# Kernel optimization log

Measured on AMD Instinct MI355X. Metric: run time of the kernel, lower is better.

The kernel has to match this reference:

```python
import jax, jax.numpy as jnp
import numpy as np
from jax import lax

B, T_Y, T_X = 16, 1600, 400
MEL_C, TXT_C, MAS_C = 80, 512, 384
HID = MAS_C * 2          # SwiGLUConvFFN hidden width (mas_channels*2)
NEG = -1e9


def setup_inputs() -> dict:
    key = jax.random.key(0)
    ks = jax.random.split(key, 20)
    p = lambda k, s: jax.random.normal(k, s, jnp.float32) * 0.02
    return {
        "mel_hidden_states": jax.random.normal(ks[0], (B, T_Y, MEL_C), jnp.float32),
        "text_hidden_states": jax.random.normal(ks[1], (B, T_X, TXT_C), jnp.float32),
        # mel SwiGLU conv-FFN (kernel 5): in->2*HID, gate, HID->MAS_C
        "mel_w1": p(ks[2], (2 * HID, MEL_C, 5)), "mel_b1": jnp.zeros((2 * HID,), jnp.float32),
        "mel_w2": p(ks[3], (MAS_C, HID, 5)),     "mel_b2": jnp.zeros((MAS_C,), jnp.float32),
        # text SwiGLU conv-FFN (kernel 3)
        "txt_w1": p(ks[4], (2 * HID, TXT_C, 3)), "txt_b1": jnp.zeros((2 * HID,), jnp.float32),
        "txt_w2": p(ks[5], (MAS_C, HID, 3)),     "txt_b2": jnp.zeros((MAS_C,), jnp.float32),
        # SimpleAttention query/key projections (value proj does not affect returned outputs)
        "wq": p(ks[6], (MAS_C, MAS_C)), "bq": jnp.zeros((MAS_C,), jnp.float32),
        "wk": p(ks[7], (MAS_C, MAS_C)), "bk": jnp.zeros((MAS_C,), jnp.float32),
        "x_lens": jax.random.randint(ks[8], (B,), T_X // 2, T_X + 1).astype(jnp.int32),
        "y_lens": jax.random.randint(ks[9], (B,), T_Y // 2, T_Y + 1).astype(jnp.int32),
    }


def _conv_ffn(x, pad_mask, w1, b1, w2, b2):
    """SwiGLU/ReGLU conv FFN. x:(B,T,C), pad_mask:(B,T) True=padded."""
    keep = (~pad_mask)[:, None, :].astype(x.dtype)          # (B,1,T)
    h = jnp.transpose(x, (0, 2, 1)) * keep                  # (B,C,T)
    dn = ("NCH", "OIH", "NCH")
    h = lax.conv_general_dilated(h, w1, (1,), "SAME", dimension_numbers=dn) + b1[None, :, None]
    a, g = jnp.split(h, 2, axis=1)
    h = a * jax.nn.relu(g) * keep                           # relugt gating
    h = lax.conv_general_dilated(h, w2, (1,), "SAME", dimension_numbers=dn) + b2[None, :, None]
    return jnp.transpose(h * keep, (0, 2, 1))               # (B,T,out)


def _mas_single(logp, t_x, t_y):
    """Glow-TTS maximum_path for one item. logp:(T_X,T_Y). Returns hard path (T_X,T_Y)."""
    xi = jnp.arange(T_X)
    yi = jnp.arange(T_Y)
    valid = (xi[:, None] < t_x) & (yi[None, :] < t_y) & (xi[:, None] <= yi[None, :])
    lp = jnp.where(valid, logp, NEG)

    def fstep(prev, col):                                   # prev:(T_X,), col:(T_X,)
        shifted = jnp.concatenate([jnp.full((1,), NEG, prev.dtype), prev[:-1]])
        cur = col + jnp.maximum(prev, shifted)
        return cur, cur

    init = jnp.where(xi == 0, 0.0, NEG).astype(logp.dtype)
    _, v = lax.scan(fstep, init, lp.T)                      # v:(T_Y,T_X) DP table

    def bstep(x, y):                                        # backtrack from y=T_Y-1 down
        active = y < t_y
        row = (xi == x) & active
        vp = v[y - 1]
        dec = (x > 0) & ((x == y) | (vp[jnp.maximum(x - 1, 0)] > vp[x]))
        new_x = jnp.where(active & (y > 0) & dec, x - 1, x)
        return new_x, row

    _, rows = lax.scan(bstep, t_x - 1, jnp.arange(T_Y - 1, -1, -1))
    return rows[::-1].T.astype(jnp.float32)                 # (T_X,T_Y)


def _safe_log(t, eps=1e-6):
    return jnp.nan_to_num(jnp.log(t + eps), nan=eps)


def reference(mel_hidden_states, text_hidden_states,
              mel_w1, mel_b1, mel_w2, mel_b2,
              txt_w1, txt_b1, txt_w2, txt_b2,
              wq, bq, wk, bk, x_lens, y_lens):
    x_mask = jnp.arange(T_X)[None, :] >= x_lens[:, None]    # (B,T_X) True=padded
    y_mask = jnp.arange(T_Y)[None, :] >= y_lens[:, None]    # (B,T_Y)

    text_proj = _conv_ffn(text_hidden_states, x_mask, txt_w1, txt_b1, txt_w2, txt_b2)
    mel_proj = _conv_ffn(mel_hidden_states, y_mask, mel_w1, mel_b1, mel_w2, mel_b2)

    q = mel_proj @ wq.T + bq                                # (B,T_Y,D)
    k = text_proj @ wk.T + bk                               # (B,T_X,D)
    scores = jnp.einsum("byd,bxd->byx", q, k) / (MAS_C ** 0.5)
    # expand_masks: mask==0 only where query AND key are both padded (faithful to source)
    both_pad = y_mask[:, :, None] & x_mask[:, None, :]
    scores = jnp.where(both_pad, jnp.float32(-1e-9), scores)
    attn_w = jax.nn.softmax(scores, axis=-1)                # (B,T_Y,T_X)

    avg_attn = attn_w[:, None]                              # (B,1,T_Y,T_X)
    attn_logprob = _safe_log(avg_attn)

    mas_in = jnp.transpose(attn_logprob[:, 0], (0, 2, 1))   # (B,T_X,T_Y)
    attn_hard = lax.stop_gradient(jax.vmap(_mas_single)(mas_in, x_lens, y_lens))
    attn_hard_dur = attn_hard.sum(2)                        # (B,T_X)
    return avg_attn, attn_logprob, attn_hard, attn_hard_dur
```

## Files before the change

kernel.cpp:

```cpp
#include <hip/hip_runtime.h>
#include <cstdint>

#define B 16
#define TY 1600
#define TX 400
#define MAS 384
#define HID 768
#define NEGV -1e9f

typedef __bf16 bf16x8 __attribute__((ext_vector_type(8)));
typedef float  f32x4  __attribute__((ext_vector_type(4)));
typedef float  f32x16 __attribute__((ext_vector_type(16)));

__device__ __forceinline__ f32x4 mfma16(bf16x8 a, bf16x8 b, f32x4 c) {
  return __builtin_amdgcn_mfma_f32_16x16x32_bf16(a, b, c, 0, 0, 0);
}
__device__ __forceinline__ f32x16 mfma32(bf16x8 a, bf16x8 b, f32x16 c) {
  return __builtin_amdgcn_mfma_f32_32x32x16_bf16(a, b, c, 0, 0, 0);
}

__global__ void split_pad_k(const float* __restrict__ in, __bf16* __restrict__ oh,
                            __bf16* __restrict__ ol, int CIN, int CINP, long n) {
  long i = (long)blockIdx.x * 256 + threadIdx.x;
  if (i >= n) return;
  long row = i / CINP; int ci = (int)(i - row * CINP);
  float v = (ci < CIN) ? in[row * CIN + ci] : 0.f;
  __bf16 h = (__bf16)v;
  oh[i] = h; ol[i] = (__bf16)(v - (float)h);
}

__global__ void wsplit_k(const float* __restrict__ w, __bf16* __restrict__ oh,
                         __bf16* __restrict__ ol, int CIN, int K_, int CINP, long n) {
  long i = (long)blockIdx.x * 256 + threadIdx.x;
  if (i >= n) return;
  long kdspan = (long)K_ * CINP;
  long nn = i / kdspan; int kd = (int)(i - nn * kdspan);
  int k = kd / CINP, ci = kd - k * CINP;
  float v = (ci < CIN) ? w[(nn * CIN + ci) * K_ + k] : 0.f;
  __bf16 h = (__bf16)v;
  oh[i] = h; ol[i] = (__bf16)(v - (float)h);
}

__global__ void tsplit_k(const float* __restrict__ in, __bf16* __restrict__ oh,
                         __bf16* __restrict__ ol, int JTOT, long n) {
  long i = (long)blockIdx.x * 256 + threadIdx.x;
  if (i >= n) return;
  int m = (int)(i / JTOT), j = (int)(i - (long)m * JTOT);
  float v = in[i];
  long o = (long)j * 384 + m;
  __bf16 h = (__bf16)v;
  oh[o] = h; ol[o] = (__bf16)(v - (float)h);
}

__global__ void fold_bias_k(const float* __restrict__ wq, const float* __restrict__ b,
                            float* __restrict__ o) {
  int n = threadIdx.x;
  float s = 0.f;
  for (int m = 0; m < 384; ++m) s = fmaf(wq[n * 384 + m], b[m], s);
  o[n] = s;
}

template<int KK>
__global__ __launch_bounds__(256)
void fold_mfma(const __bf16* __restrict__ xh, const __bf16* __restrict__ xl,
               const __bf16* __restrict__ wh, const __bf16* __restrict__ wl,
               __bf16* __restrict__ oh, __bf16* __restrict__ ol)
{
  constexpr int CINP = 384, ROWS = 64, STRIDE = 65;
  __shared__ float4 xs[8 * STRIDE];
  const int t0 = blockIdx.x * 64, n0 = blockIdx.y * 128;
  const int tid = threadIdx.x, wn = tid >> 6, lane = tid & 63;
  const int lr = lane & 15, lg = lane >> 4;
  const f32x4 Z4 = {0.f, 0.f, 0.f, 0.f};
  f32x4 acc[4][2];
  #pragma unroll
  for (int m = 0; m < 4; ++m) { acc[m][0] = Z4; acc[m][1] = Z4; }

  #pragma unroll 1
  for (int ci0 = 0; ci0 < CINP; ci0 += 32) {
    __syncthreads();
    for (int e = tid; e < ROWS * 8; e += 256) {
      int row = e >> 3, sc = e & 7, spl = sc >> 2, cg = sc & 3;
      int t = t0 + row;
      xs[(spl * 4 + cg) * STRIDE + row] =
          *(const float4*)((spl ? xl : xh) + (size_t)t * CINP + ci0 + cg * 8);
    }
    __syncthreads();
    bf16x8 ah[4], al[4];
    #pragma unroll
    for (int mf = 0; mf < 4; ++mf) {
      int row = mf * 16 + lr;
      ah[mf] = *(const bf16x8*)&xs[lg * STRIDE + row];
      al[mf] = *(const bf16x8*)&xs[(4 + lg) * STRIDE + row];
    }
    size_t kd = (size_t)ci0 + lg * 8;
    bf16x8 bh[2], bl[2];
    #pragma unroll
    for (int nf = 0; nf < 2; ++nf) {
      int nc = n0 + wn * 32 + nf * 16 + lr;
      bh[nf] = *(const bf16x8*)(wh + (size_t)nc * 384 + kd);
      bl[nf] = *(const bf16x8*)(wl + (size_t)nc * 384 + kd);
    }
    #pragma unroll
    for (int nf = 0; nf < 2; ++nf)
      #pragma unroll
      for (int mf = 0; mf < 4; ++mf) acc[mf][nf] = mfma16(ah[mf], bh[nf], acc[mf][nf]);
    #pragma unroll
    for (int nf = 0; nf < 2; ++nf)
      #pragma unroll
      for (int mf = 0; mf < 4; ++mf) acc[mf][nf] = mfma16(ah[mf], bl[nf], acc[mf][nf]);
    #pragma unroll
    for (int nf = 0; nf < 2; ++nf)
      #pragma unroll
      for (int mf = 0; mf < 4; ++mf) acc[mf][nf] = mfma16(al[mf], bh[nf], acc[mf][nf]);
  }
  #pragma unroll
  for (int nf = 0; nf < 2; ++nf) {
    int c = n0 + wn * 32 + nf * 16 + lr;
    #pragma unroll
    for (int mf = 0; mf < 4; ++mf) {
      #pragma unroll
      for (int r = 0; r < 4; ++r) {
        int j = t0 + mf * 16 + lg * 4 + r;
        int k = j % KK, ci = j / KK;
        size_t o = (size_t)((((ci >> 4) * KK + k) * 2 + ((ci >> 3) & 1)) * 3072)
                 + (size_t)c * 8 + (ci & 7);
        float v = acc[mf][nf][r];
        __bf16 vh = (__bf16)v;
        oh[o] = vh; ol[o] = (__bf16)(v - (float)vh);
      }
    }
  }
}

template<int CINP, int K, int T>
__global__ __launch_bounds__(256)
void conv1_mfma(const __bf16* __restrict__ xh, const __bf16* __restrict__ xl,
                const __bf16* __restrict__ wh, const __bf16* __restrict__ wl,
                const float* __restrict__ bias, const int* __restrict__ lens,
                __bf16* __restrict__ hh, __bf16* __restrict__ hl)
{
  constexpr int BM = 128, PAD = K / 2, ROWS = BM + K - 1, KD = K * CINP;
  __shared__ float4 xs[8 * ROWS];
  const int b = blockIdx.z, t0 = blockIdx.x * BM, n0 = blockIdx.y * 64;
  const int tid = threadIdx.x, wid = tid >> 6, lane = tid & 63;
  const int wm = wid >> 1, wn = wid & 1, lr = lane & 15, lg = lane >> 4;
  const int len = lens[b];
  const f32x4 Z4 = {0.f, 0.f, 0.f, 0.f};
  f32x4 acc_a[4][2], acc_g[4][2];
  #pragma unroll
  for (int m = 0; m < 4; ++m)
    #pragma unroll
    for (int n = 0; n < 2; ++n) { acc_a[m][n] = Z4; acc_g[m][n] = Z4; }

  #pragma unroll 1
  for (int ci0 = 0; ci0 < CINP; ci0 += 32) {
    __syncthreads();
    for (int e = tid; e < ROWS * 8; e += 256) {
      int row = e >> 3, sc = e & 7, spl = sc >> 2, cg = sc & 3;
      int t = t0 + row - PAD;
      float4 v = {0.f, 0.f, 0.f, 0.f};
      if (t >= 0 && t < len)
        v = *(const float4*)((spl ? xl : xh) + ((size_t)b * T + t) * CINP + ci0 + cg * 8);
      xs[(spl * 4 + cg) * ROWS + row] = v;
    }
    __syncthreads();
    #pragma unroll
    for (int k = 0; k < K; ++k) {
      bf16x8 ah[4], al[4];
      #pragma unroll
      for (int mf = 0; mf < 4; ++mf) {
        int row = wm * 64 + mf * 16 + lr + k;
        ah[mf] = *(const bf16x8*)&xs[lg * ROWS + row];
        al[mf] = *(const bf16x8*)&xs[(4 + lg) * ROWS + row];
      }
      size_t kd = (size_t)k * CINP + ci0 + lg * 8;
      #pragma unroll
      for (int nf = 0; nf < 2; ++nf) {
        int na = n0 + wn * 32 + nf * 16 + lr;
        bf16x8 bah = *(const bf16x8*)(wh + (size_t)na * KD + kd);
        bf16x8 bal = *(const bf16x8*)(wl + (size_t)na * KD + kd);
        bf16x8 bgh = *(const bf16x8*)(wh + (size_t)(na + HID) * KD + kd);
        bf16x8 bgl = *(const bf16x8*)(wl + (size_t)(na + HID) * KD + kd);
        #pragma unroll
        for (int mf = 0; mf < 4; ++mf) {
          acc_a[mf][nf] = mfma16(ah[mf], bah, acc_a[mf][nf]);
          acc_a[mf][nf] = mfma16(ah[mf], bal, acc_a[mf][nf]);
          acc_a[mf][nf] = mfma16(al[mf], bah, acc_a[mf][nf]);
          acc_g[mf][nf] = mfma16(ah[mf], bgh, acc_g[mf][nf]);
          acc_g[mf][nf] = mfma16(ah[mf], bgl, acc_g[mf][nf]);
          acc_g[mf][nf] = mfma16(al[mf], bgh, acc_g[mf][nf]);
        }
      }
    }
  }
  #pragma unroll
  for (int nf = 0; nf < 2; ++nf) {
    int c = n0 + wn * 32 + nf * 16 + lr;
    float ba = bias[c], bg = bias[c + HID];
    #pragma unroll
    for (int mf = 0; mf < 4; ++mf) {
      #pragma unroll
      for (int r = 0; r < 4; ++r) {
        int t = t0 + wm * 64 + mf * 16 + lg * 4 + r;
        if (t < T) {
          float a = acc_a[mf][nf][r] + ba;
          float g = acc_g[mf][nf][r] + bg;
          float v = a * fmaxf(g, 0.f);
          __bf16 vh = (__bf16)v;
          size_t o = ((size_t)b * T + t) * HID + c;
          hh[o] = vh;
          hl[o] = (__bf16)(v - (float)vh);
        }
      }
    }
  }
}

template<int K, int T, bool STORET>
__global__ __launch_bounds__(256)
void conv2_mfma(const __bf16* __restrict__ xh, const __bf16* __restrict__ xl,
                const __bf16* __restrict__ wh, const __bf16* __restrict__ wl,
                const float* __restrict__ bias, const float* __restrict__ ab,
                const int* __restrict__ lens, float* __restrict__ out)
{
  constexpr int CINP = 768, BM = 128, PAD = K / 2, ROWS = BM + K - 1, STRIDE = ROWS + 1;
  constexpr int BROWS = K * 2;
  __shared__ float4 xa[4 * STRIDE];
  __shared__ float4 bs[2 * BROWS * 192];
  const int b = blockIdx.z, t0 = blockIdx.x * BM, n0 = blockIdx.y * 192;
  const int tid = threadIdx.x, wid = tid >> 6, lane = tid & 63;
  const int wm = wid >> 1, wn = wid & 1, lc = lane & 31, lk = lane >> 5;
  const int len = lens[b];
  f32x16 acc[2][3];
  #pragma unroll
  for (int m = 0; m < 2; ++m)
    #pragma unroll
    for (int n = 0; n < 3; ++n)
      #pragma unroll
      for (int r = 0; r < 16; ++r) acc[m][n][r] = 0.f;

  #pragma unroll 1
  for (int s = 0; s < 48; ++s) {
    __syncthreads();
    for (int e = tid; e < ROWS * 4; e += 256) {
      int row = e >> 2, sc = e & 3, spl = sc >> 1, cg = sc & 1;
      int t = t0 + row - PAD;
      float4 v = {0.f, 0.f, 0.f, 0.f};
      if (t >= 0 && t < len)
        v = *(const float4*)((spl ? xl : xh) + ((size_t)b * T + t) * CINP + s * 16 + cg * 8);
      xa[(spl * 2 + cg) * STRIDE + row] = v;
    }
    for (int r = wid; r < 2 * BROWS; r += 4) {
      int spl = r / BROWS, rr = r - spl * BROWS;
      const char* src = (const char*)((spl ? wl : wh) + (size_t)(s * BROWS + rr) * 3072
                                      + (size_t)n0 * 8) + (size_t)lane * 16;
      char* dst = (char*)&bs[r * 192];
      #pragma unroll
      for (int i = 0; i < 3; ++i)
        __builtin_amdgcn_global_load_lds(
            (const __attribute__((address_space(1))) void*)(src + i * 1024),
            (__attribute__((address_space(3))) void*)(dst + i * 1024), 16, 0, 0);
    }
    __syncthreads();
    #pragma unroll
    for (int k = 0; k < K; ++k) {
      bf16x8 ah[2], al[2], bh[3], bl[3];
      #pragma unroll
      for (int mf = 0; mf < 2; ++mf) {
        int row = wm * 64 + mf * 32 + lc + k;
        ah[mf] = *(const bf16x8*)&xa[lk * STRIDE + row];
        al[mf] = *(const bf16x8*)&xa[(2 + lk) * STRIDE + row];
      }
      #pragma unroll
      for (int nf = 0; nf < 3; ++nf) {
        int col = wn * 96 + nf * 32 + lc;
        bh[nf] = *(const bf16x8*)&bs[(k * 2 + lk) * 192 + col];
        bl[nf] = *(const bf16x8*)&bs[(BROWS + k * 2 + lk) * 192 + col];
      }
      #pragma unroll
      for (int nf = 0; nf < 3; ++nf)
        #pragma unroll
        for (int mf = 0; mf < 2; ++mf)
          acc[mf][nf] = mfma32(ah[mf], bh[nf], acc[mf][nf]);
      #pragma unroll
      for (int nf = 0; nf < 3; ++nf)
        #pragma unroll
        for (int mf = 0; mf < 2; ++mf)
          acc[mf][nf] = mfma32(ah[mf], bl[nf], acc[mf][nf]);
      #pragma unroll
      for (int nf = 0; nf < 3; ++nf)
        #pragma unroll
        for (int mf = 0; mf < 2; ++mf)
          acc[mf][nf] = mfma32(al[mf], bh[nf], acc[mf][nf]);
    }
  }
  #pragma unroll
  for (int nf = 0; nf < 3; ++nf) {
    int c = n0 + wn * 96 + nf * 32 + lc;
    float bb = bias[c], aB = ab[c];
    #pragma unroll
    for (int mf = 0; mf < 2; ++mf) {
      #pragma unroll
      for (int r = 0; r < 16; ++r) {
        int t = t0 + wm * 64 + mf * 32 + (r & 3) + 8 * (r >> 2) + 4 * lk;
        if (t < T) {
          float v = acc[mf][nf][r] + bb;
          if (t >= len) v = 0.f;
          v += aB;
          if (STORET) out[((size_t)b * MAS + c) * T + t] = v;
          else        out[((size_t)b * T + t) * MAS + c] = v;
        }
      }
    }
  }
}

__global__ __launch_bounds__(512)
void scores_k(const float* __restrict__ q, const float* __restrict__ kT,
              const int* __restrict__ xl, const int* __restrict__ yl,
              float* __restrict__ oattn, float* __restrict__ ologp)
{
  __shared__ float qs[16 * 384];
  __shared__ float tmp[8];
  const int b = blockIdx.y, y0 = blockIdx.x * 16, tid = threadIdx.x;
  for (int e = tid; e < 16 * 384; e += 512)
    qs[e] = q[((size_t)b * TY + (y0 + e / 384)) * 384 + (e - (e / 384) * 384)];
  __syncthreads();
  float acc[16];
  #pragma unroll
  for (int i = 0; i < 16; ++i) acc[i] = 0.f;
  const int x = tid;
  if (x < TX) {
    const float* kb = kT + (size_t)b * MAS * TX + x;
    for (int d = 0; d < 384; d += 4) {
      float k0 = kb[(size_t)(d + 0) * TX], k1 = kb[(size_t)(d + 1) * TX];
      float k2 = kb[(size_t)(d + 2) * TX], k3 = kb[(size_t)(d + 3) * TX];
      #pragma unroll
      for (int yy = 0; yy < 16; ++yy) {
        float4 qv = *(const float4*)&qs[yy * 384 + d];
        acc[yy] = fmaf(qv.x, k0, fmaf(qv.y, k1, fmaf(qv.z, k2, fmaf(qv.w, k3, acc[yy]))));
      }
    }
  }
  const int xlen = xl[b], ylen = yl[b];
  const float scale = 0.05103103630798288f;
  const bool xpad = (x >= xlen);
  const int wv = tid >> 6, ln = tid & 63;
  #pragma unroll 1
  for (int yy = 0; yy < 16; ++yy) {
    int y = y0 + yy;
    float s = -3.0e38f;
    if (x < TX) {
      s = acc[yy] * scale;
      if (xpad && (y >= ylen)) s = -1e-9f;
    }
    float m = s;
    for (int off = 32; off; off >>= 1) m = fmaxf(m, __shfl_xor(m, off));
    if (ln == 0) tmp[wv] = m;
    __syncthreads();
    float mx = fmaxf(fmaxf(fmaxf(tmp[0], tmp[1]), fmaxf(tmp[2], tmp[3])),
                     fmaxf(fmaxf(tmp[4], tmp[5]), fmaxf(tmp[6], tmp[7])));
    __syncthreads();
    float e = (x < TX) ? expf(s - mx) : 0.f;
    float sm = e;
    for (int off = 32; off; off >>= 1) sm += __shfl_xor(sm, off);
    if (ln == 0) tmp[wv] = sm;
    __syncthreads();
    float tot = tmp[0] + tmp[1] + tmp[2] + tmp[3] + tmp[4] + tmp[5] + tmp[6] + tmp[7];
    __syncthreads();
    if (x < TX) {
      float w = e / tot;
      size_t o = ((size_t)b * TY + y) * TX + x;
      oattn[o] = w;
      ologp[o] = logf(w + 1e-6f);
    }
  }
}

#define MAS_LD(blkv, buf) do {                                           \
    int base_ = (blkv) * 4;                                              \
    _Pragma("unroll")                                                    \
    for (int d_ = 0; d_ < 4; ++d_) {                                     \
      int yr_ = base_ + d_; if (yr_ > TY - 1) yr_ = TY - 1;              \
      const float* r_ = lpb + (size_t)yr_ * TX;                          \
      buf[d_ * 3 + 0] = *(const float4*)(r_ + lb0);                      \
      buf[d_ * 3 + 1] = *(const float4*)(r_ + lb1);                      \
      buf[d_ * 3 + 2] = *(const float4*)(r_ + lb2);                      \
    } } while (0)

#define MAS_BLK(blkv, buf) do {                                          \
    float h0 = __shfl_up(w[8], 1),  h1 = __shfl_up(w[9], 1);             \
    float h2 = __shfl_up(w[10], 1), h3 = __shfl_up(w[11], 1);            \
    w[0] = lane ? h0 : NEGV; w[1] = lane ? h1 : NEGV;                    \
    w[2] = lane ? h2 : NEGV; w[3] = lane ? h3 : NEGV;                    \
    const int y0_ = (blkv) * 4;                                          \
    const bool ph1_ = (y0_ < TX);                                        \
    _Pragma("unroll")                                                    \
    for (int d_ = 0; d_ < 4; ++d_) {                                     \
      const int y_ = y0_ + d_;                                           \
      float lp[12];                                                      \
      _Pragma("unroll")                                                  \
      for (int k_ = 0; k_ < 3; ++k_) {                                   \
        float4 v_ = buf[d_ * 3 + k_];                                    \
        lp[k_*4+0] = v_.x + wxm[k_*4+0]; lp[k_*4+1] = v_.y + wxm[k_*4+1];\
        lp[k_*4+2] = v_.z + wxm[k_*4+2]; lp[k_*4+3] = v_.w + wxm[k_*4+3];\
      }                                                                  \
      if (ph1_) {                                                        \
        int c_ = y_ - p0;                                                \
        _Pragma("unroll")                                                \
        for (int i_ = 0; i_ < 12; ++i_) lp[i_] = (i_ <= c_) ? lp[i_] : NEGV; \
      }                                                                  \
      unsigned byte_ = 0;                                                \
      _Pragma("unroll")                                                  \
      for (int j_ = 0; j_ < 8; ++j_)                                     \
        byte_ |= (w[j_ + 3] > w[j_ + 4]) ? (1u << j_) : 0u;              \
      float nw[12];                                                      \
      nw[0] = lp[0] + w[0];                                              \
      _Pragma("unroll")                                                  \
      for (int i_ = 1; i_ < 12; ++i_) nw[i_] = lp[i_] + fmaxf(w[i_], w[i_ - 1]); \
      bb[(size_t)y_ * 64 + lane] = (unsigned char)byte_;                 \
      _Pragma("unroll")                                                  \
      for (int i_ = 0; i_ < 12; ++i_) w[i_] = nw[i_];                    \
    } } while (0)

__global__ __launch_bounds__(64)
void mas_fwd(const float* __restrict__ logprob, const int* __restrict__ xl,
             const int* __restrict__ yl, unsigned char* __restrict__ bits)
{
  const int b = blockIdx.x;
  const int lane = threadIdx.x;
  const int xlen = xl[b], ylen = yl[b];
  const float* lpb = logprob + (size_t)b * TY * TX;
  unsigned char* bb = bits + (size_t)b * TY * 64;
  const int p0 = lane * 8 - 4;
  int t;
  t = p0;     if (t < 0) t = 0; if (t > 396) t = 396; const int lb0 = t;
  t = p0 + 4; if (t < 0) t = 0; if (t > 396) t = 396; const int lb1 = t;
  t = p0 + 8; if (t < 0) t = 0; if (t > 396) t = 396; const int lb2 = t;

  float w[12], wxm[12];
  #pragma unroll
  for (int i = 0; i < 12; ++i) {
    int p = p0 + i;
    wxm[i] = (p >= 0 && p < xlen) ? 0.f : NEGV;
    w[i] = (p == 0) ? 0.f : NEGV;
  }

  float4 bufA[12], bufB[12];
  MAS_LD(0, bufA);
  MAS_LD(1, bufB);
  const int nblk = (ylen + 3) >> 2;
  int blk = 0;
  #pragma unroll 1
  for (; blk + 1 < nblk; blk += 2) {
    MAS_BLK(blk, bufA);
    MAS_LD(blk + 2, bufA);
    MAS_BLK(blk + 1, bufB);
    MAS_LD(blk + 3, bufB);
  }
  if (blk < nblk) MAS_BLK(blk, bufA);
}

__global__ __launch_bounds__(64)
void mas_bt(const unsigned char* __restrict__ bits, const int* __restrict__ xl,
            const int* __restrict__ yl, float* __restrict__ hard, float* __restrict__ dur)
{
  const int b = blockIdx.x;
  const int lane = threadIdx.x;
  const int xlen = xl[b], ylen = yl[b];
  const unsigned char* bb = bits + (size_t)b * TY * 64;
  float* hb = hard + (size_t)b * TX * TY;
  float* db = dur + (size_t)b * TX;

  int x = xlen - 1;
  int cnt = 0;
  #pragma unroll 1
  for (int ycur = ylen - 1; ycur >= 0; ycur -= 64) {
    int lo = x - 63; if (lo < 0) lo = 0;
    const int wb = (lo >> 3) & ~3;
    int ry = ycur - lane;
    unsigned w0 = 0, w1 = 0, w2 = 0;
    if (ry >= 0) {
      const unsigned* rp = (const unsigned*)(bb + (size_t)ry * 64 + wb);
      w0 = rp[0]; w1 = rp[1]; w2 = rp[2];
    }
    const int rows = (ycur + 1 < 64) ? (ycur + 1) : 64;
    #pragma unroll 1
    for (int s = 0; s < rows; s += 8) {
      const int cnt8 = (rows - s < 8) ? (rows - s) : 8;
      unsigned r0[8], r1[8], r2[8];
      #pragma unroll
      for (int u = 0; u < 8; ++u) {
        r0[u] = (unsigned)__builtin_amdgcn_readlane((int)w0, s + u);
        r1[u] = (unsigned)__builtin_amdgcn_readlane((int)w1, s + u);
        r2[u] = (unsigned)__builtin_amdgcn_readlane((int)w2, s + u);
      }
      #pragma unroll
      for (int u = 0; u < 8; ++u) {
        if (u < cnt8) {
          const int yy = ycur - s - u;
          ++cnt;
          if (yy > 0 && x > 0) {
            const int boff = (x >> 3) - wb;
            const unsigned word = (boff < 4) ? r0[u] : ((boff < 8) ? r1[u] : r2[u]);
            const unsigned byte = word >> ((boff & 3) * 8);
            if ((x == yy) || ((byte >> (x & 7)) & 1)) {
              for (int q = lane; q < cnt; q += 64) hb[(size_t)x * TY + yy + q] = 1.0f;
              if (lane == 0) db[x] = (float)cnt;
              cnt = 0;
              --x;
            }
          }
        }
      }
    }
  }
  for (int q = lane; q < cnt; q += 64) hb[(size_t)x * TY + q] = 1.0f;
  if (lane == 0) db[x] = (float)cnt;
}

extern "C" void kernel_launch(void* const* d_in, const int* in_sizes, int n_in,
                              void* d_out, int out_size, void* d_ws, size_t ws_size,
                              hipStream_t stream) {
  const float* mel_x  = (const float*)d_in[0];
  const float* txt_x  = (const float*)d_in[1];
  const float* mel_w1 = (const float*)d_in[2];
  const float* mel_b1 = (const float*)d_in[3];
  const float* mel_w2 = (const float*)d_in[4];
  const float* mel_b2 = (const float*)d_in[5];
  const float* txt_w1 = (const float*)d_in[6];
  const float* txt_b1 = (const float*)d_in[7];
  const float* txt_w2 = (const float*)d_in[8];
  const float* txt_b2 = (const float*)d_in[9];
  const float* wq     = (const float*)d_in[10];
  const float* bq     = (const float*)d_in[11];
  const float* wk     = (const float*)d_in[12];
  const float* bk     = (const float*)d_in[13];
  const int*   xl     = (const int*)d_in[14];
  const int*   yl     = (const int*)d_in[15];

  char* wsb = (char*)d_ws;
  constexpr size_t MXH   = 0;
  constexpr size_t MXL   = MXH   + 4915200;
  constexpr size_t TXH   = MXL   + 4915200;
  constexpr size_t TXL   = TXH   + 6553600;
  constexpr size_t KTF   = TXH;
  constexpr size_t WFMH  = TXL   + 6553600;
  constexpr size_t WFML  = WFMH  + 2949120;
  constexpr size_t WFTH  = WFML  + 2949120;
  constexpr size_t WFTL  = WFTH  + 1769472;
  constexpr size_t B2M   = WFTL  + 1769472;
  constexpr size_t B2T   = B2M   + 2048;
  constexpr size_t HH    = B2T   + 2048;
  constexpr size_t HL    = HH    + 39321600;
  constexpr size_t BITS  = MXH;
  constexpr size_t SCR   = HL    + 39321600;
  constexpr size_t W1MH  = SCR;
  constexpr size_t W1ML  = W1MH  + 1474560;
  constexpr size_t W1TH  = W1ML  + 1474560;
  constexpr size_t W1TL  = W1TH  + 4718592;
  constexpr size_t WQH   = W1TL  + 4718592;
  constexpr size_t WQL   = WQH   + 294912;
  constexpr size_t WKH   = WQL   + 294912;
  constexpr size_t WKL   = WKH   + 294912;
  constexpr size_t W2TMH = WKL   + 294912;
  constexpr size_t W2TML = W2TMH + 2949120;
  constexpr size_t W2TTH = W2TML + 2949120;
  constexpr size_t W2TTL = W2TTH + 1769472;
  constexpr size_t QF    = SCR;

  float* out = (float*)d_out;
  float* o_attn = out;
  float* o_logp = out + (size_t)10240000;
  float* o_hard = out + (size_t)20480000;
  float* o_dur  = out + (size_t)30720000;

  hipMemsetAsync(o_hard, 0, (size_t)(10240000 + 6400) * sizeof(float), stream);

  split_pad_k<<<9600, 256, 0, stream>>>(mel_x, (__bf16*)(wsb + MXH), (__bf16*)(wsb + MXL), 80, 96, 2457600L);
  split_pad_k<<<12800, 256, 0, stream>>>(txt_x, (__bf16*)(wsb + TXH), (__bf16*)(wsb + TXL), 512, 512, 3276800L);
  wsplit_k<<<2880, 256, 0, stream>>>(mel_w1, (__bf16*)(wsb + W1MH), (__bf16*)(wsb + W1ML), 80, 5, 96, 737280L);
  wsplit_k<<<9216, 256, 0, stream>>>(txt_w1, (__bf16*)(wsb + W1TH), (__bf16*)(wsb + W1TL), 512, 3, 512, 2359296L);
  wsplit_k<<<576, 256, 0, stream>>>(wq, (__bf16*)(wsb + WQH), (__bf16*)(wsb + WQL), 384, 1, 384, 147456L);
  wsplit_k<<<576, 256, 0, stream>>>(wk, (__bf16*)(wsb + WKH), (__bf16*)(wsb + WKL), 384, 1, 384, 147456L);
  tsplit_k<<<5760, 256, 0, stream>>>(mel_w2, (__bf16*)(wsb + W2TMH), (__bf16*)(wsb + W2TML), 3840, 1474560L);
  tsplit_k<<<3456, 256, 0, stream>>>(txt_w2, (__bf16*)(wsb + W2TTH), (__bf16*)(wsb + W2TTL), 2304, 884736L);
  fold_mfma<5><<<dim3(60, 3), 256, 0, stream>>>(
      (const __bf16*)(wsb + W2TMH), (const __bf16*)(wsb + W2TML),
      (const __bf16*)(wsb + WQH), (const __bf16*)(wsb + WQL),
      (__bf16*)(wsb + WFMH), (__bf16*)(wsb + WFML));
  fold_mfma<3><<<dim3(36, 3), 256, 0, stream>>>(
      (const __bf16*)(wsb + W2TTH), (const __bf16*)(wsb + W2TTL),
      (const __bf16*)(wsb + WKH), (const __bf16*)(wsb + WKL),
      (__bf16*)(wsb + WFTH), (__bf16*)(wsb + WFTL));
  fold_bias_k<<<1, 384, 0, stream>>>(wq, mel_b2, (float*)(wsb + B2M));
  fold_bias_k<<<1, 384, 0, stream>>>(wk, txt_b2, (float*)(wsb + B2T));

  conv1_mfma<512, 3, 400><<<dim3(4, 12, B), 256, 0, stream>>>(
      (const __bf16*)(wsb + TXH), (const __bf16*)(wsb + TXL),
      (const __bf16*)(wsb + W1TH), (const __bf16*)(wsb + W1TL),
      txt_b1, xl, (__bf16*)(wsb + HH), (__bf16*)(wsb + HL));
  conv2_mfma<3, 400, true><<<dim3(4, 2, B), 256, 0, stream>>>(
      (const __bf16*)(wsb + HH), (const __bf16*)(wsb + HL),
      (const __bf16*)(wsb + WFTH), (const __bf16*)(wsb + WFTL),
      (const float*)(wsb + B2T), bk, xl, (float*)(wsb + KTF));

  conv1_mfma<96, 5, 1600><<<dim3(13, 12, B), 256, 0, stream>>>(
      (const __bf16*)(wsb + MXH), (const __bf16*)(wsb + MXL),
      (const __bf16*)(wsb + W1MH), (const __bf16*)(wsb + W1ML),
      mel_b1, yl, (__bf16*)(wsb + HH), (__bf16*)(wsb + HL));
  conv2_mfma<5, 1600, false><<<dim3(13, 2, B), 256, 0, stream>>>(
      (const __bf16*)(wsb + HH), (const __bf16*)(wsb + HL),
      (const __bf16*)(wsb + WFMH), (const __bf16*)(wsb + WFML),
      (const float*)(wsb + B2M), bq, yl, (float*)(wsb + QF));

  scores_k<<<dim3(100, B), 512, 0, stream>>>(
      (const float*)(wsb + QF), (const float*)(wsb + KTF), xl, yl, o_attn, o_logp);
  mas_fwd<<<B, 64, 0, stream>>>(o_logp, xl, yl, (unsigned char*)(wsb + BITS));
  mas_bt<<<B, 64, 0, stream>>>((const unsigned char*)(wsb + BITS), xl, yl, o_hard, o_dur);
}
```

Baseline: 1.574 ms.

## Fuse MAS forward and backtrack kernels, batch bit stores, deepen prefetch

```diff
diff --git a/kernel.cpp b/kernel.cpp
--- a/kernel.cpp
+++ b/kernel.cpp
@@ -389,7 +389,7 @@
       buf[d_ * 3 + 2] = *(const float4*)(r_ + lb2);                      \
     } } while (0)
 
-#define MAS_BLK(blkv, buf) do {                                          \
+#define MAS_BLK(blkv, buf, PAR) do {                                     \
     float h0 = __shfl_up(w[8], 1),  h1 = __shfl_up(w[9], 1);             \
     float h2 = __shfl_up(w[10], 1), h3 = __shfl_up(w[11], 1);            \
     w[0] = lane ? h0 : NEGV; w[1] = lane ? h1 : NEGV;                    \
@@ -415,24 +415,29 @@
       _Pragma("unroll")                                                  \
       for (int j_ = 0; j_ < 8; ++j_)                                     \
         byte_ |= (w[j_ + 3] > w[j_ + 4]) ? (1u << j_) : 0u;              \
+      bitsacc |= (unsigned long long)byte_ << (((PAR) * 4 + d_) * 8);    \
       float nw[12];                                                      \
       nw[0] = lp[0] + w[0];                                              \
       _Pragma("unroll")                                                  \
       for (int i_ = 1; i_ < 12; ++i_) nw[i_] = lp[i_] + fmaxf(w[i_], w[i_ - 1]); \
-      bb[(size_t)y_ * 64 + lane] = (unsigned char)byte_;                 \
       _Pragma("unroll")                                                  \
       for (int i_ = 0; i_ < 12; ++i_) w[i_] = nw[i_];                    \
     } } while (0)
 
-__global__ __launch_bounds__(64)
-void mas_fwd(const float* __restrict__ logprob, const int* __restrict__ xl,
-             const int* __restrict__ yl, unsigned char* __restrict__ bits)
+#define MAS_ST(oddblk) do {                                              \
+    *(unsigned long long*)(bb8 + ((size_t)((oddblk) >> 1)) * 512 + (size_t)lane * 8) = bitsacc; \
+    bitsacc = 0ULL; } while (0)
+
+__global__ __launch_bounds__(64, 1)
+void mas_k(const float* __restrict__ logprob, const int* __restrict__ xl,
+           const int* __restrict__ yl, unsigned char* __restrict__ bits,
+           float* __restrict__ hard, float* __restrict__ dur)
 {
   const int b = blockIdx.x;
   const int lane = threadIdx.x;
   const int xlen = xl[b], ylen = yl[b];
   const float* lpb = logprob + (size_t)b * TY * TX;
-  unsigned char* bb = bits + (size_t)b * TY * 64;
+  unsigned char* bb8 = bits + (size_t)b * 102400;
   const int p0 = lane * 8 - 4;
   int t;
   t = p0;     if (t < 0) t = 0; if (t > 396) t = 396; const int lb0 = t;
@@ -447,34 +452,40 @@
     w[i] = (p == 0) ? 0.f : NEGV;
   }
 
-  float4 bufA[12], bufB[12];
-  MAS_LD(0, bufA);
-  MAS_LD(1, bufB);
+  float4 buf0[12], buf1[12], buf2[12], buf3[12];
+  MAS_LD(0, buf0); MAS_LD(1, buf1); MAS_LD(2, buf2); MAS_LD(3, buf3);
+  unsigned long long bitsacc = 0ULL;
   const int nblk = (ylen + 3) >> 2;
   int blk = 0;
   #pragma unroll 1
-  for (; blk + 1 < nblk; blk += 2) {
-    MAS_BLK(blk, bufA);
-    MAS_LD(blk + 2, bufA);
-    MAS_BLK(blk + 1, bufB);
-    MAS_LD(blk + 3, bufB);
-  }
-  if (blk < nblk) MAS_BLK(blk, bufA);
-}
-
-__global__ __launch_bounds__(64)
-void mas_bt(const unsigned char* __restrict__ bits, const int* __restrict__ xl,
-            const int* __restrict__ yl, float* __restrict__ hard, float* __restrict__ dur)
-{
-  const int b = blockIdx.x;
-  const int lane = threadIdx.x;
-  const int xlen = xl[b], ylen = yl[b];
-  const unsigned char* bb = bits + (size_t)b * TY * 64;
+  for (; blk + 3 < nblk; blk += 4) {
+    __builtin_amdgcn_sched_barrier(0);
+    MAS_BLK(blk, buf0, 0);     MAS_LD(blk + 4, buf0);
+    __builtin_amdgcn_sched_barrier(0);
+    MAS_BLK(blk + 1, buf1, 1); MAS_LD(blk + 5, buf1); MAS_ST(blk + 1);
+    __builtin_amdgcn_sched_barrier(0);
+    MAS_BLK(blk + 2, buf2, 0); MAS_LD(blk + 6, buf2);
+    __builtin_amdgcn_sched_barrier(0);
+    MAS_BLK(blk + 3, buf3, 1); MAS_LD(blk + 7, buf3); MAS_ST(blk + 3);
+  }
+  {
+    const int r = nblk - blk;
+    if (r > 0) MAS_BLK(blk, buf0, 0);
+    if (r > 1) { MAS_BLK(blk + 1, buf1, 1); MAS_ST(blk + 1); }
+    if (r > 2) MAS_BLK(blk + 2, buf2, 0);
+    if (r == 1 || r == 3) {
+      *(unsigned long long*)(bb8 + ((size_t)((blk + r - 1) >> 1)) * 512 + (size_t)lane * 8) = bitsacc;
+    }
+  }
+
+  __threadfence();
+  __syncthreads();
+
+  int x = xlen - 1;
+  int cnt = 0;
   float* hb = hard + (size_t)b * TX * TY;
   float* db = dur + (size_t)b * TX;
 
-  int x = xlen - 1;
-  int cnt = 0;
   #pragma unroll 1
   for (int ycur = ylen - 1; ycur >= 0; ycur -= 64) {
     int lo = x - 63; if (lo < 0) lo = 0;
@@ -482,8 +493,13 @@
     int ry = ycur - lane;
     unsigned w0 = 0, w1 = 0, w2 = 0;
     if (ry >= 0) {
-      const unsigned* rp = (const unsigned*)(bb + (size_t)ry * 64 + wb);
-      w0 = rp[0]; w1 = rp[1]; w2 = rp[2];
+      const unsigned char* p = bb8 + (size_t)(ry >> 3) * 512 + (ry & 7);
+      unsigned bt_[12];
+      #pragma unroll
+      for (int j = 0; j < 12; ++j) bt_[j] = p[(size_t)(wb + j) * 8];
+      w0 = bt_[0] | (bt_[1] << 8) | (bt_[2] << 16) | (bt_[3] << 24);
+      w1 = bt_[4] | (bt_[5] << 8) | (bt_[6] << 16) | (bt_[7] << 24);
+      w2 = bt_[8] | (bt_[9] << 8) | (bt_[10] << 16) | (bt_[11] << 24);
     }
     const int rows = (ycur + 1 < 64) ? (ycur + 1) : 64;
     #pragma unroll 1
@@ -617,6 +633,5 @@
 
   scores_k<<<dim3(100, B), 512, 0, stream>>>(
       (const float*)(wsb + QF), (const float*)(wsb + KTF), xl, yl, o_attn, o_logp);
-  mas_fwd<<<B, 64, 0, stream>>>(o_logp, xl, yl, (unsigned char*)(wsb + BITS));
-  mas_bt<<<B, 64, 0, stream>>>((const unsigned char*)(wsb + BITS), xl, yl, o_hard, o_dur);
-}
+  mas_k<<<B, 64, 0, stream>>>(o_logp, xl, yl, (unsigned char*)(wsb + BITS), o_hard, o_dur);
+}
```

Result: no change. 1.555 ms (-1.2%).
